# Kernel optimization log

Measured on AMD Instinct MI355X. Metric: run time of the kernel, lower is better.

Reference implementation:

```python
import jax, jax.numpy as jnp
import numpy as np

B, L, DIM, H = 1, 2048, 3072, 24
D = DIM // H  # 128
EPS = 1e-6

def setup_inputs() -> dict:
    key = jax.random.key(0)
    ks = jax.random.split(key, 7)
    x = jax.random.normal(ks[0], (B, L, DIM), dtype=jnp.float32)
    pe = jax.random.normal(ks[1], (B, 1, L, D // 2, 2, 2), dtype=jnp.float32)
    w_qkv = jax.random.normal(ks[2], (DIM, 3 * DIM), dtype=jnp.float32) / np.sqrt(DIM)
    q_scale = jnp.ones((D,), dtype=jnp.float32)
    k_scale = jnp.ones((D,), dtype=jnp.float32)
    w_proj = jax.random.normal(ks[3], (DIM, DIM), dtype=jnp.float32) / np.sqrt(DIM)
    b_proj = jnp.zeros((DIM,), dtype=jnp.float32)
    return {"x": x, "pe": pe, "w_qkv": w_qkv, "q_scale": q_scale,
            "k_scale": k_scale, "w_proj": w_proj, "b_proj": b_proj}

def _rmsnorm(t, scale):
    # flax nn.RMSNorm: t * rsqrt(mean(t^2, -1) + eps) * scale
    ms = jnp.mean(jnp.square(t), axis=-1, keepdims=True)
    return t * jax.lax.rsqrt(ms + EPS) * scale

def _apply_rope(xq, xk, pe):
    # xq/xk: [B,H,L,D]; pe: [B,1,L,D/2,2,2]
    xq_ = xq.reshape(*xq.shape[:-1], -1, 1, 2)
    xk_ = xk.reshape(*xk.shape[:-1], -1, 1, 2)
    xq_out = pe[..., 0] * xq_[..., 0] + pe[..., 1] * xq_[..., 1]
    xk_out = pe[..., 0] * xk_[..., 0] + pe[..., 1] * xk_[..., 1]
    return xq_out.reshape(xq.shape), xk_out.reshape(xk.shape)

def reference(x, pe, w_qkv, q_scale, k_scale, w_proj, b_proj):
    qkv = jnp.einsum('bld,de->ble', x, w_qkv)            # [B,L,3*DIM]
    qkv = qkv.reshape(B, L, 3, H, D)
    qkv = jnp.moveaxis(qkv, 2, 0)                          # [3,B,H?,..]
    q, k, v = jnp.transpose(qkv, (0, 1, 3, 2, 4))          # each [B,H,L,D]
    q = _rmsnorm(q, q_scale).astype(v.dtype)
    k = _rmsnorm(k, k_scale).astype(v.dtype)
    q, k = _apply_rope(q, k, pe)
    scale = 1.0 / np.sqrt(D)
    scores = jnp.einsum('bhqd,bhkd->bhqk', q, k) * scale   # [B,H,L,L]
    attn = jax.nn.softmax(scores, axis=-1)
    out = jnp.einsum('bhqk,bhkd->bhqd', attn, v)           # [B,H,L,D]
    out = jnp.transpose(out, (0, 2, 1, 3)).reshape(B, L, DIM)
    return jnp.einsum('bld,de->ble', out, w_proj) + b_proj
```

## Files before the change

kernel.cpp:

```cpp
#include <hip/hip_runtime.h>

#define L_    2048
#define DIM_  3072
#define H_    24
#define D_    128
#define NQKV  9216

typedef __attribute__((ext_vector_type(8))) short bf16x8;
typedef __attribute__((ext_vector_type(4))) short bf16x4;
typedef __attribute__((ext_vector_type(4))) float f32x4;

__device__ __forceinline__ unsigned short f2bf(float f) {
  union { float f; unsigned u; } v; v.f = f;
  unsigned r = v.u + 0x7fffu + ((v.u >> 16) & 1u);
  return (unsigned short)(r >> 16);
}

__device__ __forceinline__ void gload_lds16(const void* g, void* l) {
  auto* lp = reinterpret_cast<__attribute__((address_space(3))) unsigned int*>(
      reinterpret_cast<uintptr_t>(l));
  auto* gp = reinterpret_cast<const __attribute__((address_space(1))) unsigned int*>(
      reinterpret_cast<uintptr_t>(g));
  __builtin_amdgcn_global_load_lds(gp, lp, 16, 0, 0);
}

__global__ void cast_f32_to_bf16(const float* __restrict__ in,
                                 unsigned short* __restrict__ out, int n) {
  int total = n >> 2;
  int stride = gridDim.x * blockDim.x;
  for (int i = blockIdx.x * blockDim.x + threadIdx.x; i < total; i += stride) {
    float4 v = ((const float4*)in)[i];
    ushort4 o;
    o.x = f2bf(v.x); o.y = f2bf(v.y); o.z = f2bf(v.z); o.w = f2bf(v.w);
    ((ushort4*)out)[i] = o;
  }
}

__global__ __launch_bounds__(256)
void castT_f32_bf16(const float* __restrict__ in, unsigned short* __restrict__ out,
                    int K, int N) {
  int k = blockIdx.x * 256 + threadIdx.x;
  int n0 = blockIdx.y * 128;
  const float* src = in + (size_t)k * N + n0;
  #pragma unroll 4
  for (int j4 = 0; j4 < 32; j4++) {
    float4 v = *(const float4*)&src[j4 * 4];
    out[(size_t)(n0 + j4 * 4 + 0) * K + k] = f2bf(v.x);
    out[(size_t)(n0 + j4 * 4 + 1) * K + k] = f2bf(v.y);
    out[(size_t)(n0 + j4 * 4 + 2) * K + k] = f2bf(v.z);
    out[(size_t)(n0 + j4 * 4 + 3) * K + k] = f2bf(v.w);
  }
}

__global__ __launch_bounds__(256, 3)
void gemm_qkv(const unsigned short* __restrict__ A,
              const unsigned short* __restrict__ Bt,
              const float* __restrict__ pe,
              const float* __restrict__ q_scale,
              const float* __restrict__ k_scale,
              unsigned short* __restrict__ Qo,
              unsigned short* __restrict__ Ko,
              unsigned short* __restrict__ Vo)
{
  const int K = DIM_;
  __shared__ unsigned short As[128 * 64];
  __shared__ unsigned short Bs[128 * 64];
  const int tid  = threadIdx.x;
  const int wave = tid >> 6;
  const int lane = tid & 63;
  const int l15  = lane & 15;
  const int quad = lane >> 4;
  const int wm = wave >> 1, wn = wave & 1;

  const int lin = blockIdx.x;
  const int st  = lin >> 6;
  const int w6  = lin & 63;
  const int bn_idx = (st >> 1) * 8 + (w6 & 7);
  const int bm_idx = (st & 1) * 8 + (w6 >> 3);
  const int bm = bm_idx * 128;
  const int bn = bn_idx * 128;

  const int srow = lane >> 3;
  const int scol = (lane & 7) ^ srow;
  const unsigned short* Ag = A  + (size_t)(bm + wave * 32 + srow) * K + scol * 8;
  const unsigned short* Bg = Bt + (size_t)(bn + wave * 32 + srow) * K + scol * 8;
  unsigned short* Al = &As[(wave * 32) * 64];
  unsigned short* Bl = &Bs[(wave * 32) * 64];

  f32x4 acc[4][4];
  #pragma unroll
  for (int i = 0; i < 4; i++)
    #pragma unroll
    for (int j = 0; j < 4; j++) acc[i][j] = (f32x4){0.f, 0.f, 0.f, 0.f};

  for (int k0 = 0; k0 < K; k0 += 64) {
    __syncthreads();
    #pragma unroll
    for (int j = 0; j < 4; j++) {
      gload_lds16(Ag + (size_t)j * 8 * K + k0, Al + j * 8 * 64);
      gload_lds16(Bg + (size_t)j * 8 * K + k0, Bl + j * 8 * 64);
    }
    __syncthreads();
    #pragma unroll
    for (int ks = 0; ks < 2; ks++) {
      const int cph = ((ks * 4 + quad) ^ (l15 & 7)) * 8;
      bf16x8 af[4], bf[4];
      #pragma unroll
      for (int mt = 0; mt < 4; mt++)
        af[mt] = *(const bf16x8*)&As[(wm * 64 + mt * 16 + l15) * 64 + cph];
      #pragma unroll
      for (int nt = 0; nt < 4; nt++)
        bf[nt] = *(const bf16x8*)&Bs[(wn * 64 + nt * 16 + l15) * 64 + cph];
      #pragma unroll
      for (int mt = 0; mt < 4; mt++)
        #pragma unroll
        for (int nt = 0; nt < 4; nt++)
          acc[mt][nt] = __builtin_amdgcn_mfma_f32_16x16x32_bf16(
              af[mt], bf[nt], acc[mt][nt], 0, 0, 0);
    }
  }
  __syncthreads();

  if (bn_idx < 48) {
    const bool isQ = bn_idx < 24;
    const int  hh  = isQ ? bn_idx : bn_idx - 24;
    const float* sc = isQ ? q_scale : k_scale;
    unsigned short* dst = isQ ? Qo : Ko;
    float* rbuf = (float*)As;
    #pragma unroll
    for (int mt = 0; mt < 4; mt++)
      #pragma unroll
      for (int r = 0; r < 4; r++) {
        float p = 0.f;
        #pragma unroll
        for (int nt = 0; nt < 4; nt++) p += acc[mt][nt][r] * acc[mt][nt][r];
        p += __shfl_xor(p, 1); p += __shfl_xor(p, 2);
        p += __shfl_xor(p, 4); p += __shfl_xor(p, 8);
        if (l15 == 0) rbuf[wn * 128 + wm * 64 + mt * 16 + quad * 4 + r] = p;
      }
    __syncthreads();
    #pragma unroll
    for (int mt = 0; mt < 4; mt++)
      #pragma unroll
      for (int r = 0; r < 4; r++) {
        const int lrow = wm * 64 + mt * 16 + quad * 4 + r;
        const int lg = bm + lrow;
        float ms = (rbuf[lrow] + rbuf[128 + lrow]) * (1.f / 128.f);
        float rinv = rsqrtf(ms + 1e-6f);
        #pragma unroll
        for (int nt = 0; nt < 4; nt++) {
          const int d = wn * 64 + nt * 16 + l15;
          float n  = acc[mt][nt][r] * rinv * sc[d];
          float np = __shfl_xor(n, 1);
          float2 ab = *(const float2*)&pe[(size_t)lg * 256 + (d >> 1) * 4 + (d & 1) * 2];
          float xe = (d & 1) ? np : n;
          float xo = (d & 1) ? n  : np;
          float o = ab.x * xe + ab.y * xo;
          if (isQ) o *= 0.08838834764831845f;
          dst[((size_t)hh * L_ + lg) * D_ + d] = f2bf(o);
        }
      }
  } else {
    const int hh = bn_idx - 48;
    #pragma unroll
    for (int mt = 0; mt < 4; mt++)
      #pragma unroll
      for (int nt = 0; nt < 4; nt++)
        #pragma unroll
        for (int r = 0; r < 4; r++) {
          int row = bm + wm * 64 + mt * 16 + quad * 4 + r;
          int col = hh * D_ + wn * 64 + nt * 16 + l15;
          Vo[(size_t)row * DIM_ + col] = f2bf(acc[mt][nt][r]);
        }
  }
}

__global__ __launch_bounds__(256, 3)
void gemm_proj_sk(const unsigned short* __restrict__ A,
                  const unsigned short* __restrict__ Bt,
                  float* __restrict__ P0, float* __restrict__ P1,
                  int M, int N, int K)
{
  __shared__ unsigned short As[128 * 64];
  __shared__ unsigned short Bs[128 * 64];
  const int tid  = threadIdx.x;
  const int wave = tid >> 6;
  const int lane = tid & 63;
  const int l15  = lane & 15;
  const int quad = lane >> 4;
  const int wm = wave >> 1, wn = wave & 1;
  const int bm = blockIdx.y * 128;
  const int bn = blockIdx.x * 128;
  const int z  = blockIdx.z;
  const int kbeg = z * (K >> 1), kend = kbeg + (K >> 1);
  float* Pout = z ? P1 : P0;

  const int srow = lane >> 3;
  const int scol = (lane & 7) ^ srow;
  const unsigned short* Ag = A  + (size_t)(bm + wave * 32 + srow) * K + scol * 8;
  const unsigned short* Bg = Bt + (size_t)(bn + wave * 32 + srow) * K + scol * 8;
  unsigned short* Al = &As[(wave * 32) * 64];
  unsigned short* Bl = &Bs[(wave * 32) * 64];

  f32x4 acc[4][4];
  #pragma unroll
  for (int i = 0; i < 4; i++)
    #pragma unroll
    for (int j = 0; j < 4; j++) acc[i][j] = (f32x4){0.f, 0.f, 0.f, 0.f};

  for (int k0 = kbeg; k0 < kend; k0 += 64) {
    __syncthreads();
    #pragma unroll
    for (int j = 0; j < 4; j++) {
      gload_lds16(Ag + (size_t)j * 8 * K + k0, Al + j * 8 * 64);
      gload_lds16(Bg + (size_t)j * 8 * K + k0, Bl + j * 8 * 64);
    }
    __syncthreads();
    #pragma unroll
    for (int ks = 0; ks < 2; ks++) {
      const int cph = ((ks * 4 + quad) ^ (l15 & 7)) * 8;
      bf16x8 af[4], bf[4];
      #pragma unroll
      for (int mt = 0; mt < 4; mt++)
        af[mt] = *(const bf16x8*)&As[(wm * 64 + mt * 16 + l15) * 64 + cph];
      #pragma unroll
      for (int nt = 0; nt < 4; nt++)
        bf[nt] = *(const bf16x8*)&Bs[(wn * 64 + nt * 16 + l15) * 64 + cph];
      #pragma unroll
      for (int mt = 0; mt < 4; mt++)
        #pragma unroll
        for (int nt = 0; nt < 4; nt++)
          acc[mt][nt] = __builtin_amdgcn_mfma_f32_16x16x32_bf16(
              af[mt], bf[nt], acc[mt][nt], 0, 0, 0);
    }
  }
  #pragma unroll
  for (int mt = 0; mt < 4; mt++)
    #pragma unroll
    for (int nt = 0; nt < 4; nt++)
      #pragma unroll
      for (int r = 0; r < 4; r++) {
        int row = bm + wm * 64 + mt * 16 + quad * 4 + r;
        int col = bn + wn * 64 + nt * 16 + l15;
        Pout[(size_t)row * N + col] = acc[mt][nt][r];
      }
}

__global__ __launch_bounds__(256)
void reduce_bias(const float* __restrict__ p0, const float* __restrict__ p1,
                 const float* __restrict__ bias, float* __restrict__ out)
{
  int col4 = blockIdx.x * 256 + threadIdx.x;
  size_t idx = (size_t)blockIdx.y * 768 + col4;
  float4 a = ((const float4*)p0)[idx];
  float4 b = ((const float4*)p1)[idx];
  float4 c = ((const float4*)bias)[col4];
  float4 o = make_float4(a.x + b.x + c.x, a.y + b.y + c.y,
                         a.z + b.z + c.z, a.w + b.w + c.w);
  ((float4*)out)[idx] = o;
}

__global__ __launch_bounds__(256)
void v_transpose(const unsigned short* __restrict__ v_buf,
                 unsigned short* __restrict__ Vt) {
  int h = blockIdx.y;
  int l = blockIdx.x * 256 + threadIdx.x;
  const unsigned short* src = v_buf + (size_t)l * DIM_ + h * D_;
  unsigned short* dst = Vt + (size_t)h * D_ * L_ + l;
  #pragma unroll
  for (int c = 0; c < 16; c++) {
    uint4 v = *(const uint4*)&src[c * 8];
    const unsigned short* pv = (const unsigned short*)&v;
    #pragma unroll
    for (int j = 0; j < 8; j++)
      dst[(size_t)(c * 8 + j) * L_] = pv[j];
  }
}

__global__ __launch_bounds__(256, 3)
void flash_attn(const unsigned short* __restrict__ Q,
                const unsigned short* __restrict__ K,
                const unsigned short* __restrict__ Vt,
                unsigned short* __restrict__ Out)
{
  __shared__ __align__(16) char smem[34304];
  unsigned short* Ks = (unsigned short*)smem;
  unsigned short* Vs = Ks + 8192;
  float*  Obuf = (float*)smem;
  float2* mlb  = (float2*)(smem + 32768);
  float4* sAr  = (float4*)(smem + 33280);

  const int tid  = threadIdx.x;
  const int wave = tid >> 6;
  const int lane = tid & 63;
  const int l15  = lane & 15;
  const int quad = lane >> 4;
  const int qg = wave >> 1;
  const int kh = wave & 1;
  const int h  = blockIdx.y;
  const int q0 = blockIdx.x * 64 + qg * 32;

  const unsigned short* Qh = Q  + (size_t)h * L_ * D_;
  const unsigned short* Kh = K  + (size_t)h * L_ * D_;
  const unsigned short* Vh = Vt + (size_t)h * D_ * L_;

  bf16x8 qf[2][4];
  #pragma unroll
  for (int nt = 0; nt < 2; nt++)
    #pragma unroll
    for (int kc = 0; kc < 4; kc++)
      qf[nt][kc] = *(const bf16x8*)&Qh[(size_t)(q0 + nt * 16 + l15) * D_ + kc * 32 + quad * 8];

  f32x4 oacc[2][8];
  #pragma unroll
  for (int i = 0; i < 2; i++)
    #pragma unroll
    for (int j = 0; j < 8; j++) oacc[i][j] = (f32x4){0.f, 0.f, 0.f, 0.f};
  float m_i[2] = {-1e30f, -1e30f}, l_i[2] = {0.f, 0.f};

  const int kr_l = lane >> 4;
  const int vr_l = lane >> 3;
  const int vcl  = (lane & 7) ^ vr_l;

  for (int t = 0; t < L_; t += 64) {
    __syncthreads();
    #pragma unroll
    for (int ji = 0; ji < 4; ji++) {
      int Rr = wave * 16 + ji * 4;
      int cl = (lane & 15) ^ ((Rr + kr_l) & 15);
      gload_lds16(&Kh[(size_t)(t + Rr + kr_l) * D_ + cl * 8], &Ks[Rr * 128]);
      int R2 = wave * 32 + ji * 8;
      gload_lds16(&Vh[(size_t)(R2 + vr_l) * L_ + t + vcl * 8], &Vs[R2 * 64]);
    }
    __syncthreads();

    f32x4 s[2][2];
    #pragma unroll
    for (int i = 0; i < 2; i++)
      #pragma unroll
      for (int j = 0; j < 2; j++) s[i][j] = (f32x4){0.f, 0.f, 0.f, 0.f};
    #pragma unroll
    for (int mt = 0; mt < 2; mt++) {
      const int krow = kh * 32 + mt * 16 + l15;
      #pragma unroll
      for (int kc = 0; kc < 4; kc++) {
        bf16x8 kf = *(const bf16x8*)&Ks[krow * 128 + (((kc * 4 + quad) ^ l15) * 8)];
        s[mt][0] = __builtin_amdgcn_mfma_f32_16x16x32_bf16(kf, qf[0][kc], s[mt][0], 0, 0, 0);
        s[mt][1] = __builtin_amdgcn_mfma_f32_16x16x32_bf16(kf, qf[1][kc], s[mt][1], 0, 0, 0);
      }
    }
    float vmax[2], alpha[2], rs[2];
    #pragma unroll
    for (int nt = 0; nt < 2; nt++) {
      vmax[nt] = fmaxf(fmaxf(fmaxf(s[0][nt][0], s[0][nt][1]), fmaxf(s[0][nt][2], s[0][nt][3])),
                       fmaxf(fmaxf(s[1][nt][0], s[1][nt][1]), fmaxf(s[1][nt][2], s[1][nt][3])));
      vmax[nt] = fmaxf(vmax[nt], __shfl_xor(vmax[nt], 16));
      vmax[nt] = fmaxf(vmax[nt], __shfl_xor(vmax[nt], 32));
      float mnew = fmaxf(m_i[nt], vmax[nt]);
      alpha[nt] = __expf(m_i[nt] - mnew);
      m_i[nt] = mnew;
      rs[nt] = 0.f;
    }
    #pragma unroll
    for (int mt = 0; mt < 2; mt++)
      #pragma unroll
      for (int nt = 0; nt < 2; nt++)
        #pragma unroll
        for (int r = 0; r < 4; r++) {
          float p = __expf(s[mt][nt][r] - m_i[nt]);
          s[mt][nt][r] = p;
          rs[nt] += p;
        }
    #pragma unroll
    for (int nt = 0; nt < 2; nt++) {
      rs[nt] += __shfl_xor(rs[nt], 16);
      rs[nt] += __shfl_xor(rs[nt], 32);
      l_i[nt] = l_i[nt] * alpha[nt] + rs[nt];
    }
    float ar[2][4];
    #pragma unroll
    for (int qt = 0; qt < 2; qt++)
      #pragma unroll
      for (int r = 0; r < 4; r++)
        ar[qt][r] = __shfl(alpha[qt], quad * 4 + r);
    #pragma unroll
    for (int qt = 0; qt < 2; qt++)
      #pragma unroll
      for (int ntd = 0; ntd < 8; ntd++)
        #pragma unroll
        for (int r = 0; r < 4; r++)
          oacc[qt][ntd][r] *= ar[qt][r];
    bf16x4 pk[2][2];
    #pragma unroll
    for (int mt = 0; mt < 2; mt++)
      #pragma unroll
      for (int qt = 0; qt < 2; qt++)
        pk[mt][qt] = (bf16x4){(short)f2bf(s[mt][qt][0]), (short)f2bf(s[mt][qt][1]),
                              (short)f2bf(s[mt][qt][2]), (short)f2bf(s[mt][qt][3])};
    #pragma unroll
    for (int ntd = 0; ntd < 8; ntd++) {
      const int vrow = ntd * 16 + l15;
      #pragma unroll
      for (int mt = 0; mt < 2; mt++) {
        int phys = (kh * 4 + mt * 2 + (quad >> 1)) ^ (l15 & 7);
        bf16x4 vf = *(const bf16x4*)&Vs[vrow * 64 + phys * 8 + (quad & 1) * 4];
        oacc[0][ntd] = __builtin_amdgcn_mfma_f32_16x16x16bf16_1k(pk[mt][0], vf, oacc[0][ntd], 0, 0, 0);
        oacc[1][ntd] = __builtin_amdgcn_mfma_f32_16x16x16bf16_1k(pk[mt][1], vf, oacc[1][ntd], 0, 0, 0);
      }
    }
  }

  __syncthreads();
  if (kh == 1) {
    #pragma unroll
    for (int qt = 0; qt < 2; qt++)
      #pragma unroll
      for (int ntd = 0; ntd < 8; ntd++)
        #pragma unroll
        for (int r = 0; r < 4; r++)
          Obuf[(size_t)(qg * 32 + qt * 16 + quad * 4 + r) * 128 + ntd * 16 + l15] = oacc[qt][ntd][r];
    if (quad == 0)
      #pragma unroll
      for (int qt = 0; qt < 2; qt++)
        mlb[qg * 32 + qt * 16 + l15] = make_float2(m_i[qt], l_i[qt]);
  }
  __syncthreads();
  if (kh == 0 && quad == 0) {
    #pragma unroll
    for (int qt = 0; qt < 2; qt++) {
      float2 m1 = mlb[qg * 32 + qt * 16 + l15];
      float M  = fmaxf(m_i[qt], m1.x);
      float a0 = __expf(m_i[qt] - M);
      float a1 = __expf(m1.x - M);
      float Ls = l_i[qt] * a0 + m1.y * a1;
      sAr[qg * 32 + qt * 16 + l15] = make_float4(a0, a1, 1.f / Ls, 0.f);
    }
  }
  __syncthreads();
  if (kh == 0) {
    #pragma unroll
    for (int qt = 0; qt < 2; qt++)
      #pragma unroll
      for (int r = 0; r < 4; r++) {
        float4 A = sAr[qg * 32 + qt * 16 + quad * 4 + r];
        #pragma unroll
        for (int ntd = 0; ntd < 8; ntd++) {
          float o1 = Obuf[(size_t)(qg * 32 + qt * 16 + quad * 4 + r) * 128 + ntd * 16 + l15];
          float v  = (oacc[qt][ntd][r] * A.x + o1 * A.y) * A.z;
          Out[(size_t)(q0 + qt * 16 + quad * 4 + r) * DIM_ + h * D_ + ntd * 16 + l15] = f2bf(v);
        }
      }
  }
}

extern "C" void kernel_launch(void* const* d_in, const int* in_sizes, int n_in,
                              void* d_out, int out_size, void* d_ws, size_t ws_size,
                              hipStream_t stream) {
  const float* x       = (const float*)d_in[0];
  const float* pe      = (const float*)d_in[1];
  const float* w_qkv   = (const float*)d_in[2];
  const float* q_scale = (const float*)d_in[3];
  const float* k_scale = (const float*)d_in[4];
  const float* w_proj  = (const float*)d_in[5];
  const float* b_proj  = (const float*)d_in[6];

  unsigned short* w_qkvT  = (unsigned short*)d_ws;
  unsigned short* w_projT = w_qkvT + 28311552;
  unsigned short* x_b     = w_projT + 9437184;
  unsigned short* v_buf   = x_b + 6291456;
  unsigned short* q_r     = v_buf + 6291456;
  unsigned short* k_r     = q_r + 6291456;
  unsigned short* vt_r    = k_r + 6291456;
  unsigned short* attn_b  = vt_r + 6291456;
  float* proj_p0 = (float*)x_b;
  float* proj_p1 = (float*)q_r;

  cast_f32_to_bf16<<<2048, 256, 0, stream>>>(x, x_b, 6291456);
  castT_f32_bf16<<<dim3(12, 72), 256, 0, stream>>>(w_qkv, w_qkvT, 3072, 9216);
  castT_f32_bf16<<<dim3(12, 24), 256, 0, stream>>>(w_proj, w_projT, 3072, 3072);

  gemm_qkv<<<1152, 256, 0, stream>>>(
      x_b, w_qkvT, pe, q_scale, k_scale, q_r, k_r, v_buf);

  v_transpose<<<dim3(8, 24), 256, 0, stream>>>(v_buf, vt_r);

  flash_attn<<<dim3(32, 24), 256, 0, stream>>>(q_r, k_r, vt_r, attn_b);

  gemm_proj_sk<<<dim3(24, 16, 2), 256, 0, stream>>>(
      attn_b, w_projT, proj_p0, proj_p1, 2048, 3072, 3072);

  reduce_bias<<<dim3(3, 2048), 256, 0, stream>>>(
      proj_p0, proj_p1, b_proj, (float*)d_out);
}
```

Baseline: 526.5 us.

## Double-buffer K tiles with async prefetch, lazy softmax rescale, and MFMA priority

Restructures the flash attention loop so the next K tile is prefetched into a second LDS buffer while the current tile is computed, and the V tile load is issued after the PV MFMAs, with fine-grained vmcnt waits instead of full syncthreads. Adds a lazy online-softmax rescale that skips the alpha multiply of the output accumulators when the running max grows by no more than 8. Wraps MFMA sections in s_setprio. LDS grows to 48KB, which may reduce occupancy below the 3-block launch bound, and the manual vmcnt counting is fragile.

```diff
diff --git a/kernel.cpp b/kernel.cpp
--- a/kernel.cpp
+++ b/kernel.cpp
@@ -283,9 +283,7 @@
                 const unsigned short* __restrict__ Vt,
                 unsigned short* __restrict__ Out)
 {
-  __shared__ __align__(16) char smem[34304];
-  unsigned short* Ks = (unsigned short*)smem;
-  unsigned short* Vs = Ks + 8192;
+  __shared__ __align__(16) char smem[49152];
   float*  Obuf = (float*)smem;
   float2* mlb  = (float2*)(smem + 32768);
   float4* sAr  = (float4*)(smem + 33280);
@@ -322,45 +320,89 @@
   const int vr_l = lane >> 3;
   const int vcl  = (lane & 7) ^ vr_l;
 
-  for (int t = 0; t < L_; t += 64) {
-    __syncthreads();
+  auto stageK = [&](int t, int b) {
+    unsigned short* Ksb = (unsigned short*)(smem + b * 16384);
     #pragma unroll
     for (int ji = 0; ji < 4; ji++) {
       int Rr = wave * 16 + ji * 4;
-      int cl = (lane & 15) ^ ((Rr + kr_l) & 15);
-      gload_lds16(&Kh[(size_t)(t + Rr + kr_l) * D_ + cl * 8], &Ks[Rr * 128]);
+      int cl = l15 ^ ((Rr + kr_l) & 15);
+      gload_lds16(&Kh[(size_t)(t + Rr + kr_l) * D_ + cl * 8], &Ksb[Rr * 128]);
+    }
+  };
+  auto stageV = [&](int t) {
+    unsigned short* Vsb = (unsigned short*)(smem + 32768);
+    #pragma unroll
+    for (int ji = 0; ji < 4; ji++) {
       int R2 = wave * 32 + ji * 8;
-      gload_lds16(&Vh[(size_t)(R2 + vr_l) * L_ + t + vcl * 8], &Vs[R2 * 64]);
-    }
-    __syncthreads();
+      gload_lds16(&Vh[(size_t)(R2 + vr_l) * L_ + t + vcl * 8], &Vsb[R2 * 64]);
+    }
+  };
+
+  stageK(0, 0);
+  stageV(0);
+
+  #pragma unroll 2
+  for (int t = 0; t < L_; t += 64) {
+    const int cur = (t >> 6) & 1;
+    const bool more = (t + 64 < L_);
+
+    asm volatile("s_waitcnt vmcnt(4)" ::: "memory");
+    __builtin_amdgcn_s_barrier();
+    if (more) stageK(t + 64, cur ^ 1);
+
+    const unsigned short* Ksc = (const unsigned short*)(smem + cur * 16384);
+    const unsigned short* Vsc = (const unsigned short*)(smem + 32768);
 
     f32x4 s[2][2];
     #pragma unroll
     for (int i = 0; i < 2; i++)
       #pragma unroll
       for (int j = 0; j < 2; j++) s[i][j] = (f32x4){0.f, 0.f, 0.f, 0.f};
+    __builtin_amdgcn_s_setprio(1);
     #pragma unroll
     for (int mt = 0; mt < 2; mt++) {
       const int krow = kh * 32 + mt * 16 + l15;
       #pragma unroll
       for (int kc = 0; kc < 4; kc++) {
-        bf16x8 kf = *(const bf16x8*)&Ks[krow * 128 + (((kc * 4 + quad) ^ l15) * 8)];
+        bf16x8 kf = *(const bf16x8*)&Ksc[krow * 128 + (((kc * 4 + quad) ^ l15) * 8)];
         s[mt][0] = __builtin_amdgcn_mfma_f32_16x16x32_bf16(kf, qf[0][kc], s[mt][0], 0, 0, 0);
         s[mt][1] = __builtin_amdgcn_mfma_f32_16x16x32_bf16(kf, qf[1][kc], s[mt][1], 0, 0, 0);
       }
     }
-    float vmax[2], alpha[2], rs[2];
+    __builtin_amdgcn_s_setprio(0);
+
+    float vmax[2];
     #pragma unroll
     for (int nt = 0; nt < 2; nt++) {
       vmax[nt] = fmaxf(fmaxf(fmaxf(s[0][nt][0], s[0][nt][1]), fmaxf(s[0][nt][2], s[0][nt][3])),
                        fmaxf(fmaxf(s[1][nt][0], s[1][nt][1]), fmaxf(s[1][nt][2], s[1][nt][3])));
       vmax[nt] = fmaxf(vmax[nt], __shfl_xor(vmax[nt], 16));
       vmax[nt] = fmaxf(vmax[nt], __shfl_xor(vmax[nt], 32));
-      float mnew = fmaxf(m_i[nt], vmax[nt]);
-      alpha[nt] = __expf(m_i[nt] - mnew);
-      m_i[nt] = mnew;
-      rs[nt] = 0.f;
-    }
+    }
+    if (!__all((vmax[0] - m_i[0] <= 8.f) && (vmax[1] - m_i[1] <= 8.f))) {
+      float alpha[2];
+      #pragma unroll
+      for (int nt = 0; nt < 2; nt++) {
+        float mnew = fmaxf(m_i[nt], vmax[nt]);
+        alpha[nt] = __expf(m_i[nt] - mnew);
+        m_i[nt] = mnew;
+        l_i[nt] *= alpha[nt];
+      }
+      float ar[2][4];
+      #pragma unroll
+      for (int qt = 0; qt < 2; qt++)
+        #pragma unroll
+        for (int r = 0; r < 4; r++)
+          ar[qt][r] = __shfl(alpha[qt], quad * 4 + r);
+      #pragma unroll
+      for (int qt = 0; qt < 2; qt++)
+        #pragma unroll
+        for (int ntd = 0; ntd < 8; ntd++)
+          #pragma unroll
+          for (int r = 0; r < 4; r++)
+            oacc[qt][ntd][r] *= ar[qt][r];
+    }
+    float rs[2] = {0.f, 0.f};
     #pragma unroll
     for (int mt = 0; mt < 2; mt++)
       #pragma unroll
@@ -375,21 +417,8 @@
     for (int nt = 0; nt < 2; nt++) {
       rs[nt] += __shfl_xor(rs[nt], 16);
       rs[nt] += __shfl_xor(rs[nt], 32);
-      l_i[nt] = l_i[nt] * alpha[nt] + rs[nt];
-    }
-    float ar[2][4];
-    #pragma unroll
-    for (int qt = 0; qt < 2; qt++)
-      #pragma unroll
-      for (int r = 0; r < 4; r++)
-        ar[qt][r] = __shfl(alpha[qt], quad * 4 + r);
-    #pragma unroll
-    for (int qt = 0; qt < 2; qt++)
-      #pragma unroll
-      for (int ntd = 0; ntd < 8; ntd++)
-        #pragma unroll
-        for (int r = 0; r < 4; r++)
-          oacc[qt][ntd][r] *= ar[qt][r];
+      l_i[nt] += rs[nt];
+    }
     bf16x4 pk[2][2];
     #pragma unroll
     for (int mt = 0; mt < 2; mt++)
@@ -397,16 +426,28 @@
       for (int qt = 0; qt < 2; qt++)
         pk[mt][qt] = (bf16x4){(short)f2bf(s[mt][qt][0]), (short)f2bf(s[mt][qt][1]),
                               (short)f2bf(s[mt][qt][2]), (short)f2bf(s[mt][qt][3])};
+
+    if (more) asm volatile("s_waitcnt vmcnt(4)" ::: "memory");
+    else      asm volatile("s_waitcnt vmcnt(0)" ::: "memory");
+    __builtin_amdgcn_s_barrier();
+
+    __builtin_amdgcn_s_setprio(1);
     #pragma unroll
     for (int ntd = 0; ntd < 8; ntd++) {
       const int vrow = ntd * 16 + l15;
       #pragma unroll
       for (int mt = 0; mt < 2; mt++) {
         int phys = (kh * 4 + mt * 2 + (quad >> 1)) ^ (l15 & 7);
-        bf16x4 vf = *(const bf16x4*)&Vs[vrow * 64 + phys * 8 + (quad & 1) * 4];
+        bf16x4 vf = *(const bf16x4*)&Vsc[vrow * 64 + phys * 8 + (quad & 1) * 4];
         oacc[0][ntd] = __builtin_amdgcn_mfma_f32_16x16x16bf16_1k(pk[mt][0], vf, oacc[0][ntd], 0, 0, 0);
         oacc[1][ntd] = __builtin_amdgcn_mfma_f32_16x16x16bf16_1k(pk[mt][1], vf, oacc[1][ntd], 0, 0, 0);
       }
+    }
+    __builtin_amdgcn_s_setprio(0);
+
+    if (more) {
+      __builtin_amdgcn_s_barrier();
+      stageV(t + 64);
     }
   }
 
```

After: 562.0 us. +6.7%, slower.

## Restructure flash attention with double-buffered K/V tiles and lazy rescaling

Applied to the files above, without the earlier changes.

The attention kernel now gives each wave its own 16 query rows and loops over the full key range, replacing the split-key scheme that needed an LDS merge at the end. K/V tiles shrink to 32 keys and are double-buffered with async global-to-LDS loads, so the next tile's load overlaps compute and each step needs only barriers rather than full syncthreads. Online-softmax rescaling is skipped unless the running max grows by more than a threshold, and MFMA sections are raised in priority with s_setprio. Occupancy is raised to 4 blocks per CU. The tradeoffs are more loop iterations and barriers per key, and lower MFMA reuse of each K/V fragment per wave.

```diff
diff --git a/kernel.cpp b/kernel.cpp
--- a/kernel.cpp
+++ b/kernel.cpp
@@ -277,180 +277,156 @@
   }
 }
 
-__global__ __launch_bounds__(256, 3)
+__global__ __launch_bounds__(256, 4)
 void flash_attn(const unsigned short* __restrict__ Q,
                 const unsigned short* __restrict__ K,
                 const unsigned short* __restrict__ Vt,
                 unsigned short* __restrict__ Out)
 {
-  __shared__ __align__(16) char smem[34304];
-  unsigned short* Ks = (unsigned short*)smem;
-  unsigned short* Vs = Ks + 8192;
-  float*  Obuf = (float*)smem;
-  float2* mlb  = (float2*)(smem + 32768);
-  float4* sAr  = (float4*)(smem + 33280);
+  __shared__ __align__(16) char smem[32768];
 
   const int tid  = threadIdx.x;
   const int wave = tid >> 6;
   const int lane = tid & 63;
   const int l15  = lane & 15;
   const int quad = lane >> 4;
-  const int qg = wave >> 1;
-  const int kh = wave & 1;
   const int h  = blockIdx.y;
-  const int q0 = blockIdx.x * 64 + qg * 32;
+  const int q0 = blockIdx.x * 64 + wave * 16;
 
   const unsigned short* Qh = Q  + (size_t)h * L_ * D_;
   const unsigned short* Kh = K  + (size_t)h * L_ * D_;
   const unsigned short* Vh = Vt + (size_t)h * D_ * L_;
 
-  bf16x8 qf[2][4];
-  #pragma unroll
-  for (int nt = 0; nt < 2; nt++)
-    #pragma unroll
-    for (int kc = 0; kc < 4; kc++)
-      qf[nt][kc] = *(const bf16x8*)&Qh[(size_t)(q0 + nt * 16 + l15) * D_ + kc * 32 + quad * 8];
-
-  f32x4 oacc[2][8];
-  #pragma unroll
-  for (int i = 0; i < 2; i++)
-    #pragma unroll
-    for (int j = 0; j < 8; j++) oacc[i][j] = (f32x4){0.f, 0.f, 0.f, 0.f};
-  float m_i[2] = {-1e30f, -1e30f}, l_i[2] = {0.f, 0.f};
+  bf16x8 qf[4];
+  #pragma unroll
+  for (int kc = 0; kc < 4; kc++)
+    qf[kc] = *(const bf16x8*)&Qh[(size_t)(q0 + l15) * D_ + kc * 32 + quad * 8];
+
+  f32x4 oacc[8];
+  #pragma unroll
+  for (int j = 0; j < 8; j++) oacc[j] = (f32x4){0.f, 0.f, 0.f, 0.f};
+  float m_i = -1e30f, l_i = 0.f;
 
   const int kr_l = lane >> 4;
-  const int vr_l = lane >> 3;
-  const int vcl  = (lane & 7) ^ vr_l;
-
-  for (int t = 0; t < L_; t += 64) {
-    __syncthreads();
-    #pragma unroll
-    for (int ji = 0; ji < 4; ji++) {
-      int Rr = wave * 16 + ji * 4;
-      int cl = (lane & 15) ^ ((Rr + kr_l) & 15);
-      gload_lds16(&Kh[(size_t)(t + Rr + kr_l) * D_ + cl * 8], &Ks[Rr * 128]);
-      int R2 = wave * 32 + ji * 8;
-      gload_lds16(&Vh[(size_t)(R2 + vr_l) * L_ + t + vcl * 8], &Vs[R2 * 64]);
-    }
-    __syncthreads();
-
-    f32x4 s[2][2];
-    #pragma unroll
-    for (int i = 0; i < 2; i++)
-      #pragma unroll
-      for (int j = 0; j < 2; j++) s[i][j] = (f32x4){0.f, 0.f, 0.f, 0.f};
+  const int vr_l = lane >> 2;
+  const int vcl  = (lane & 3) ^ (vr_l & 3);
+
+  auto stageK = [&](int t, int b) {
+    unsigned short* Kb = (unsigned short*)(smem + b * 8192);
+    #pragma unroll
+    for (int ji = 0; ji < 2; ji++) {
+      int R0 = wave * 8 + ji * 4;
+      int R  = R0 + kr_l;
+      int c  = l15 ^ (R & 15);
+      gload_lds16(&Kh[(size_t)(t + R) * D_ + c * 8], &Kb[R0 * 128]);
+    }
+  };
+  auto stageV = [&](int t, int b) {
+    unsigned short* Vb = (unsigned short*)(smem + 16384 + b * 8192);
+    #pragma unroll
+    for (int ji = 0; ji < 2; ji++) {
+      int R0 = wave * 32 + ji * 16;
+      int R  = R0 + vr_l;
+      gload_lds16(&Vh[(size_t)R * L_ + t + vcl * 8], &Vb[R0 * 32]);
+    }
+  };
+
+  stageK(0, 0);
+  stageV(0, 0);
+
+  for (int t = 0; t < L_; t += 32) {
+    const int cur  = (t >> 5) & 1;
+    const bool more = (t + 32 < L_);
+
+    if (more) {
+      stageK(t + 32, cur ^ 1);
+      stageV(t + 32, cur ^ 1);
+      asm volatile("s_waitcnt vmcnt(4)" ::: "memory");
+    } else {
+      asm volatile("s_waitcnt vmcnt(0)" ::: "memory");
+    }
+    __builtin_amdgcn_s_barrier();
+
+    const unsigned short* Ksc = (const unsigned short*)(smem + cur * 8192);
+    const unsigned short* Vsc = (const unsigned short*)(smem + 16384 + cur * 8192);
+
+    f32x4 s[2];
+    s[0] = (f32x4){0.f, 0.f, 0.f, 0.f};
+    s[1] = (f32x4){0.f, 0.f, 0.f, 0.f};
+    __builtin_amdgcn_s_setprio(1);
     #pragma unroll
     for (int mt = 0; mt < 2; mt++) {
-      const int krow = kh * 32 + mt * 16 + l15;
+      const int krow = mt * 16 + l15;
       #pragma unroll
       for (int kc = 0; kc < 4; kc++) {
-        bf16x8 kf = *(const bf16x8*)&Ks[krow * 128 + (((kc * 4 + quad) ^ l15) * 8)];
-        s[mt][0] = __builtin_amdgcn_mfma_f32_16x16x32_bf16(kf, qf[0][kc], s[mt][0], 0, 0, 0);
-        s[mt][1] = __builtin_amdgcn_mfma_f32_16x16x32_bf16(kf, qf[1][kc], s[mt][1], 0, 0, 0);
-      }
-    }
-    float vmax[2], alpha[2], rs[2];
-    #pragma unroll
-    for (int nt = 0; nt < 2; nt++) {
-      vmax[nt] = fmaxf(fmaxf(fmaxf(s[0][nt][0], s[0][nt][1]), fmaxf(s[0][nt][2], s[0][nt][3])),
-                       fmaxf(fmaxf(s[1][nt][0], s[1][nt][1]), fmaxf(s[1][nt][2], s[1][nt][3])));
-      vmax[nt] = fmaxf(vmax[nt], __shfl_xor(vmax[nt], 16));
-      vmax[nt] = fmaxf(vmax[nt], __shfl_xor(vmax[nt], 32));
-      float mnew = fmaxf(m_i[nt], vmax[nt]);
-      alpha[nt] = __expf(m_i[nt] - mnew);
-      m_i[nt] = mnew;
-      rs[nt] = 0.f;
-    }
+        bf16x8 kf = *(const bf16x8*)&Ksc[krow * 128 + (((kc * 4 + quad) ^ l15) * 8)];
+        s[mt] = __builtin_amdgcn_mfma_f32_16x16x32_bf16(kf, qf[kc], s[mt], 0, 0, 0);
+      }
+    }
+    __builtin_amdgcn_s_setprio(0);
+
+    float vmax = fmaxf(fmaxf(fmaxf(s[0][0], s[0][1]), fmaxf(s[0][2], s[0][3])),
+                       fmaxf(fmaxf(s[1][0], s[1][1]), fmaxf(s[1][2], s[1][3])));
+    vmax = fmaxf(vmax, __shfl_xor(vmax, 16));
+    vmax = fmaxf(vmax, __shfl_xor(vmax, 32));
+    if (!__all(vmax - m_i <= 8.f)) {
+      float mnew = fmaxf(m_i, vmax);
+      float alpha = __expf(m_i - mnew);
+      m_i = mnew;
+      l_i *= alpha;
+      float ar[4];
+      #pragma unroll
+      for (int r = 0; r < 4; r++) ar[r] = __shfl(alpha, quad * 4 + r);
+      #pragma unroll
+      for (int ntd = 0; ntd < 8; ntd++)
+        #pragma unroll
+        for (int r = 0; r < 4; r++) oacc[ntd][r] *= ar[r];
+    }
+    float rs = 0.f;
     #pragma unroll
     for (int mt = 0; mt < 2; mt++)
       #pragma unroll
-      for (int nt = 0; nt < 2; nt++)
-        #pragma unroll
-        for (int r = 0; r < 4; r++) {
-          float p = __expf(s[mt][nt][r] - m_i[nt]);
-          s[mt][nt][r] = p;
-          rs[nt] += p;
-        }
-    #pragma unroll
-    for (int nt = 0; nt < 2; nt++) {
-      rs[nt] += __shfl_xor(rs[nt], 16);
-      rs[nt] += __shfl_xor(rs[nt], 32);
-      l_i[nt] = l_i[nt] * alpha[nt] + rs[nt];
-    }
-    float ar[2][4];
-    #pragma unroll
-    for (int qt = 0; qt < 2; qt++)
-      #pragma unroll
-      for (int r = 0; r < 4; r++)
-        ar[qt][r] = __shfl(alpha[qt], quad * 4 + r);
-    #pragma unroll
-    for (int qt = 0; qt < 2; qt++)
-      #pragma unroll
-      for (int ntd = 0; ntd < 8; ntd++)
-        #pragma unroll
-        for (int r = 0; r < 4; r++)
-          oacc[qt][ntd][r] *= ar[qt][r];
-    bf16x4 pk[2][2];
+      for (int r = 0; r < 4; r++) {
+        float p = __expf(s[mt][r] - m_i);
+        s[mt][r] = p;
+        rs += p;
+      }
+    rs += __shfl_xor(rs, 16);
+    rs += __shfl_xor(rs, 32);
+    l_i += rs;
+
+    bf16x4 pk[2];
     #pragma unroll
     for (int mt = 0; mt < 2; mt++)
-      #pragma unroll
-      for (int qt = 0; qt < 2; qt++)
-        pk[mt][qt] = (bf16x4){(short)f2bf(s[mt][qt][0]), (short)f2bf(s[mt][qt][1]),
-                              (short)f2bf(s[mt][qt][2]), (short)f2bf(s[mt][qt][3])};
+      pk[mt] = (bf16x4){(short)f2bf(s[mt][0]), (short)f2bf(s[mt][1]),
+                        (short)f2bf(s[mt][2]), (short)f2bf(s[mt][3])};
+
+    __builtin_amdgcn_s_setprio(1);
     #pragma unroll
     for (int ntd = 0; ntd < 8; ntd++) {
-      const int vrow = ntd * 16 + l15;
+      const int drow = ntd * 16 + l15;
       #pragma unroll
       for (int mt = 0; mt < 2; mt++) {
-        int phys = (kh * 4 + mt * 2 + (quad >> 1)) ^ (l15 & 7);
-        bf16x4 vf = *(const bf16x4*)&Vs[vrow * 64 + phys * 8 + (quad & 1) * 4];
-        oacc[0][ntd] = __builtin_amdgcn_mfma_f32_16x16x16bf16_1k(pk[mt][0], vf, oacc[0][ntd], 0, 0, 0);
-        oacc[1][ntd] = __builtin_amdgcn_mfma_f32_16x16x16bf16_1k(pk[mt][1], vf, oacc[1][ntd], 0, 0, 0);
-      }
-    }
-  }
-
-  __syncthreads();
-  if (kh == 1) {
-    #pragma unroll
-    for (int qt = 0; qt < 2; qt++)
-      #pragma unroll
-      for (int ntd = 0; ntd < 8; ntd++)
-        #pragma unroll
-        for (int r = 0; r < 4; r++)
-          Obuf[(size_t)(qg * 32 + qt * 16 + quad * 4 + r) * 128 + ntd * 16 + l15] = oacc[qt][ntd][r];
-    if (quad == 0)
-      #pragma unroll
-      for (int qt = 0; qt < 2; qt++)
-        mlb[qg * 32 + qt * 16 + l15] = make_float2(m_i[qt], l_i[qt]);
-  }
-  __syncthreads();
-  if (kh == 0 && quad == 0) {
-    #pragma unroll
-    for (int qt = 0; qt < 2; qt++) {
-      float2 m1 = mlb[qg * 32 + qt * 16 + l15];
-      float M  = fmaxf(m_i[qt], m1.x);
-      float a0 = __expf(m_i[qt] - M);
-      float a1 = __expf(m1.x - M);
-      float Ls = l_i[qt] * a0 + m1.y * a1;
-      sAr[qg * 32 + qt * 16 + l15] = make_float4(a0, a1, 1.f / Ls, 0.f);
-    }
-  }
-  __syncthreads();
-  if (kh == 0) {
-    #pragma unroll
-    for (int qt = 0; qt < 2; qt++)
-      #pragma unroll
-      for (int r = 0; r < 4; r++) {
-        float4 A = sAr[qg * 32 + qt * 16 + quad * 4 + r];
-        #pragma unroll
-        for (int ntd = 0; ntd < 8; ntd++) {
-          float o1 = Obuf[(size_t)(qg * 32 + qt * 16 + quad * 4 + r) * 128 + ntd * 16 + l15];
-          float v  = (oacc[qt][ntd][r] * A.x + o1 * A.y) * A.z;
-          Out[(size_t)(q0 + qt * 16 + quad * 4 + r) * DIM_ + h * D_ + ntd * 16 + l15] = f2bf(v);
-        }
-      }
-  }
+        int pch = (mt * 2 + (quad >> 1)) ^ (l15 & 3);
+        bf16x4 vf = *(const bf16x4*)&Vsc[drow * 32 + pch * 8 + (quad & 1) * 4];
+        oacc[ntd] = __builtin_amdgcn_mfma_f32_16x16x16bf16_1k(pk[mt], vf, oacc[ntd], 0, 0, 0);
+      }
+    }
+    __builtin_amdgcn_s_setprio(0);
+
+    __builtin_amdgcn_s_barrier();
+  }
+
+  float rinv = 1.f / l_i;
+  float lr[4];
+  #pragma unroll
+  for (int r = 0; r < 4; r++) lr[r] = __shfl(rinv, quad * 4 + r);
+  #pragma unroll
+  for (int r = 0; r < 4; r++)
+    #pragma unroll
+    for (int ntd = 0; ntd < 8; ntd++)
+      Out[(size_t)(q0 + quad * 4 + r) * DIM_ + h * D_ + ntd * 16 + l15] =
+          f2bf(oacc[ntd][r] * lr[r]);
 }
 
 extern "C" void kernel_launch(void* const* d_in, const int* in_sizes, int n_in,
```

Result: slower. 591.5 us (+12.3%).
